# Kernel tuning notes

Measured on AMD Instinct MI355X. Metric: run time of the kernel, lower is better.

The kernel has to match this reference:

```python
import jax, jax.numpy as jnp
import numpy as np

D_MODEL = 1024
N_HEADS = 16
D_KEYS = 64
D_LLM = 4096
Q_RANK = 512
KV_RANK = 512
EPS = 1e-5


def layernorm(x, g, b):
    mu = jnp.mean(x, axis=-1, keepdims=True)
    var = jnp.mean(jnp.square(x - mu), axis=-1, keepdims=True)
    return (x - mu) * jax.lax.rsqrt(var + EPS) * g + b


def setup_inputs() -> dict:
    key = jax.random.key(0)
    ks = jax.random.split(key, 10)
    te = jax.random.normal(ks[0], (4, 1024, D_MODEL), jnp.float32)
    se = jax.random.normal(ks[1], (1000, D_LLM), jnp.float32)
    s = 0.02
    return {
        'target_embedding': te,
        'source_embedding': se,
        'value_embedding': se,  # module asserts source == value
        'q_a_w': jax.random.normal(ks[2], (Q_RANK, D_MODEL), jnp.float32) * s,
        'q_ln_g': jnp.ones((Q_RANK,), jnp.float32),
        'q_ln_b': jnp.zeros((Q_RANK,), jnp.float32),
        'q_b_w': jax.random.normal(ks[3], (N_HEADS * D_KEYS, Q_RANK), jnp.float32) * s,
        'kv_a_w': jax.random.normal(ks[4], (KV_RANK, D_LLM), jnp.float32) * s,
        'kv_ln_g': jnp.ones((KV_RANK,), jnp.float32),
        'kv_ln_b': jnp.zeros((KV_RANK,), jnp.float32),
        'kv_b_w': jax.random.normal(ks[5], (N_HEADS * 2 * D_KEYS, KV_RANK), jnp.float32) * s,
        'out_w': jax.random.normal(ks[6], (D_LLM, N_HEADS * D_KEYS), jnp.float32) * s,
        'out_b': jnp.zeros((D_LLM,), jnp.float32),
    }


def reference(target_embedding, source_embedding, value_embedding,
              q_a_w, q_ln_g, q_ln_b, q_b_w,
              kv_a_w, kv_ln_g, kv_ln_b, kv_b_w, out_w, out_b):
    B, L, _ = target_embedding.shape
    S = source_embedding.shape[0]
    # Q path: LoRA down -> LN -> up, [B,L,H,E]
    q = layernorm(target_embedding @ q_a_w.T, q_ln_g, q_ln_b) @ q_b_w.T
    q = q.reshape(B, L, N_HEADS, D_KEYS)
    # KV path (no batch dim, broadcast across B)
    ckv = layernorm(source_embedding @ kv_a_w.T, kv_ln_g, kv_ln_b)  # [S, r]
    kv = (ckv @ kv_b_w.T).reshape(S, N_HEADS, 2 * D_KEYS)
    k, v = kv[..., :D_KEYS], kv[..., D_KEYS:]  # [S,H,E] each
    scale = 1.0 / np.sqrt(D_KEYS)
    scores = jnp.einsum('blhe,she->bhls', q, k)  # [B,H,L,S]
    A = jax.nn.softmax(scale * scores, axis=-1)  # dropout inactive (eval)
    out = jnp.einsum('bhls,she->blhe', A, v).reshape(B, L, N_HEADS * D_KEYS)
    return out @ out_w.T + out_b
```

## Files before the change

kernel.cpp:

```cpp
#include <hip/hip_runtime.h>

typedef unsigned short u16;
typedef __bf16 bf16x8 __attribute__((ext_vector_type(8)));
typedef __bf16 bf16x4 __attribute__((ext_vector_type(4)));
typedef float f32x4 __attribute__((ext_vector_type(4)));

#define DEV __device__ __forceinline__

DEV u16 f2bf(float f){
  unsigned u = __float_as_uint(f);
  u += 0x7fff + ((u >> 16) & 1);
  return (u16)(u >> 16);
}
DEV float bf2f(u16 v){ return __uint_as_float(((unsigned)v) << 16); }

DEV void gll16(const void* g, void* l){
  __builtin_amdgcn_global_load_lds(
    (__attribute__((address_space(1))) unsigned int*)(unsigned long long)g,
    (__attribute__((address_space(3))) unsigned int*)(unsigned int)(unsigned long long)l,
    16, 0, 0);
}

template<int WM, int WN, int OBF, int BIAS>
__global__ __launch_bounds__(256) void gemm_bt(
    const u16* __restrict__ A, int lda, long sA1, long sA2,
    const u16* __restrict__ B, int ldb, long sB1, long sB2,
    void* __restrict__ Cv, int ldc, long sC1, long sC2,
    const float* __restrict__ bias,
    int M, int N, int K, int Z2)
{
  constexpr int BM = WM*64, BN = WN*64;
  constexpr int NW = WM*WN;
  constexpr int A_INSTS = BM/16, B_INSTS = BN/16;
  constexpr int APW = A_INSTS/NW, BPW = B_INSTS/NW;
  __shared__ u16 sA[BM*32];
  __shared__ u16 sB[BN*32];
  const int tid  = threadIdx.x;
  const int wave = tid >> 6, lane = tid & 63;
  const int quad = lane >> 4, l16 = lane & 15;
  const int wm = wave % WM, wn = wave / WM;
  const long bm = blockIdx.y, bn = blockIdx.x;
  const int z  = blockIdx.z;
  const int z1 = z / Z2, z2 = z - z1*Z2;
  const u16* Ab = A + z1*sA1 + z2*sA2 + bm*BM*(long)lda;
  const u16* Bb = B + z1*sB1 + z2*sB2 + bn*BN*(long)ldb;

  f32x4 acc[4][4] = {};

  for (int k0 = 0; k0 < K; k0 += 32){
    __syncthreads();
#pragma unroll
    for (int j = 0; j < APW; j++){
      const int inst = wave*APW + j;
      const int o = inst*1024 + lane*16;
      const int row = o >> 6, colb = o & 63;
      gll16(Ab + (long)row*lda + k0 + (colb >> 1), &sA[inst*512]);
    }
#pragma unroll
    for (int j = 0; j < BPW; j++){
      const int inst = wave*BPW + j;
      const int o = inst*1024 + lane*16;
      const int row = o >> 6, colb = o & 63;
      gll16(Bb + (long)row*ldb + k0 + (colb >> 1), &sB[inst*512]);
    }
    __syncthreads();
    bf16x8 af[4], bfr[4];
#pragma unroll
    for (int mi = 0; mi < 4; mi++)
      af[mi] = *(const bf16x8*)&sA[(wm*64 + mi*16 + l16)*32 + quad*8];
#pragma unroll
    for (int ni = 0; ni < 4; ni++)
      bfr[ni] = *(const bf16x8*)&sB[(wn*64 + ni*16 + l16)*32 + quad*8];
#pragma unroll
    for (int mi = 0; mi < 4; mi++)
#pragma unroll
      for (int ni = 0; ni < 4; ni++)
        acc[mi][ni] = __builtin_amdgcn_mfma_f32_16x16x32_bf16(af[mi], bfr[ni], acc[mi][ni], 0, 0, 0);
  }

  const long crow0 = bm*BM + wm*64 + quad*4;
  const long ccol0 = bn*BN + wn*64 + l16;
  if (OBF){
    u16* Cp = (u16*)Cv + z1*sC1 + z2*sC2;
#pragma unroll
    for (int mi = 0; mi < 4; mi++)
#pragma unroll
      for (int ni = 0; ni < 4; ni++)
#pragma unroll
        for (int r = 0; r < 4; r++)
          Cp[(crow0 + mi*16 + r)*ldc + ccol0 + ni*16] = f2bf(acc[mi][ni][r]);
  } else {
    float* Cp = (float*)Cv + z1*sC1 + z2*sC2;
    float bv[4] = {0.f,0.f,0.f,0.f};
    if (BIAS){
#pragma unroll
      for (int ni = 0; ni < 4; ni++) bv[ni] = bias[ccol0 + ni*16];
    }
#pragma unroll
    for (int mi = 0; mi < 4; mi++)
#pragma unroll
      for (int ni = 0; ni < 4; ni++)
#pragma unroll
        for (int r = 0; r < 4; r++)
          Cp[(crow0 + mi*16 + r)*ldc + ccol0 + ni*16] = acc[mi][ni][r] + bv[ni];
  }
}

__global__ __launch_bounds__(512, 2) void gemm256(
    const u16* __restrict__ A, const u16* __restrict__ B,
    float* __restrict__ C, const float* __restrict__ bias,
    int N, int K, int TN)
{
  __shared__ __align__(16) u16 sA[32768];
  __shared__ __align__(16) u16 sB[32768];
  const int tid  = threadIdx.x;
  const int w    = tid >> 6, lane = tid & 63;
  const int quad = lane >> 4, l16 = lane & 15;
  const int wm = w >> 2, wn = w & 3;
  const int cpx = gridDim.x >> 3;
  const int bid = blockIdx.x;
  const int wg  = (bid & 7)*cpx + (bid >> 3);
  const long bm = wg / TN, bn = wg % TN;
  const int NT = K >> 6;

  const int rsub = lane >> 3;
  const int kk16 = (lane & 7) ^ rsub;
  const u16* Ag = A + (bm*256 + w*8 + rsub)*(long)K + kk16*8;
  const u16* Bg = B + (bn*256 + w*8 + rsub)*(long)K + kk16*8;
  u16* dA = sA + w*512;
  u16* dB = sB + w*512;

  auto stage = [&](const u16* G, u16* D, int T){
#pragma unroll
    for (int c = 0; c < 4; c++)
      gll16(G + ((long)c*64)*K + T*64, D + c*4096);
  };

  const int xr  = l16 & 7;
  const int ko0 = ((0*4 + quad) ^ xr) * 8;
  const int ko1 = ((1*4 + quad) ^ xr) * 8;
  const u16* rA0 = sA + (wm*128 + l16)*64;
  const u16* rB0 = sB + (wn*64  + l16)*64;

  f32x4 acc[8][4] = {};
  bf16x8 aF[4][2], bF[4][2];

  stage(Ag, dA, 0);
  stage(Bg, dB, 0);
  asm volatile("s_waitcnt vmcnt(0)" ::: "memory");
  __builtin_amdgcn_s_barrier();

  for (int T = 0; T < NT; ++T){
    const int buf = T & 1;
    const u16* rA = rA0 + buf*16384;
    const u16* rB = rB0 + buf*16384;

    if (T+1 < NT){
      stage(Ag, dA + (buf^1)*16384, T+1);
      stage(Bg, dB + (buf^1)*16384, T+1);
    }

#pragma unroll
    for (int nj = 0; nj < 4; nj++){
      bF[nj][0] = *(const bf16x8*)(rB + nj*1024 + ko0);
      bF[nj][1] = *(const bf16x8*)(rB + nj*1024 + ko1);
    }
#pragma unroll
    for (int mi = 0; mi < 4; mi++){
      aF[mi][0] = *(const bf16x8*)(rA + mi*1024 + ko0);
      aF[mi][1] = *(const bf16x8*)(rA + mi*1024 + ko1);
    }
#pragma unroll
    for (int kk = 0; kk < 2; kk++)
#pragma unroll
      for (int mi = 0; mi < 4; mi++)
#pragma unroll
        for (int nj = 0; nj < 4; nj++)
          acc[mi][nj] = __builtin_amdgcn_mfma_f32_16x16x32_bf16(aF[mi][kk], bF[nj][kk], acc[mi][nj], 0,0,0);

#pragma unroll
    for (int mi = 0; mi < 4; mi++){
      aF[mi][0] = *(const bf16x8*)(rA + (4+mi)*1024 + ko0);
      aF[mi][1] = *(const bf16x8*)(rA + (4+mi)*1024 + ko1);
    }
#pragma unroll
    for (int kk = 0; kk < 2; kk++)
#pragma unroll
      for (int mi = 0; mi < 4; mi++)
#pragma unroll
        for (int nj = 0; nj < 4; nj++)
          acc[4+mi][nj] = __builtin_amdgcn_mfma_f32_16x16x32_bf16(aF[mi][kk], bF[nj][kk], acc[4+mi][nj], 0,0,0);

    asm volatile("s_waitcnt vmcnt(0)" ::: "memory");
    __syncthreads();
  }

  const long crow0 = bm*256 + wm*128 + quad*4;
  const long ccol0 = bn*256 + wn*64  + l16;
  float bv[4];
#pragma unroll
  for (int ni = 0; ni < 4; ni++) bv[ni] = bias ? bias[ccol0 + ni*16] : 0.f;
#pragma unroll
  for (int mi = 0; mi < 8; mi++)
#pragma unroll
    for (int ni = 0; ni < 4; ni++)
#pragma unroll
      for (int r = 0; r < 4; r++)
        C[(crow0 + mi*16 + r)*(long)N + ccol0 + ni*16] = acc[mi][ni][r] + bv[ni];
}

__global__ __launch_bounds__(256) void cvt_all(
    const float* __restrict__ te,   const float* __restrict__ qaw,
    const float* __restrict__ qbw,  const float* __restrict__ kvaw,
    const float* __restrict__ kvbw, const float* __restrict__ outw,
    const float* __restrict__ se,
    u16* __restrict__ te_bf, u16* __restrict__ qa_bf, u16* __restrict__ qb_bf,
    u16* __restrict__ kva_bf, u16* __restrict__ kvb_bf,
    u16* __restrict__ outw_bf, u16* __restrict__ se_bf)
{
  const long NG = 4194304;
  const float QSC = 0.18033688011f;
  for (long g = (long)blockIdx.x*256 + threadIdx.x; g < NG; g += (long)gridDim.x*256){
    const float* src; u16* dst; long rel; bool zero = false; float sc = 1.f;
    if (g < 1048576)      { src=te;   dst=te_bf;   rel=g; }
    else if (g < 1179648) { src=qaw;  dst=qa_bf;   rel=g-1048576; }
    else if (g < 1310720) { src=qbw;  dst=qb_bf;   rel=g-1179648; sc = QSC; }
    else if (g < 1835008) { src=kvaw; dst=kva_bf;  rel=g-1310720; }
    else if (g < 2097152) { src=kvbw; dst=kvb_bf;  rel=g-1835008; }
    else if (g < 3145728) { src=outw; dst=outw_bf; rel=g-2097152; }
    else                  { src=se;   dst=se_bf;   rel=g-3145728; zero = (rel>>10) >= 1000; }
    ushort4 o;
    if (!zero){
      float4 v = *(const float4*)(src + rel*4);
      o.x = f2bf(v.x*sc); o.y = f2bf(v.y*sc); o.z = f2bf(v.z*sc); o.w = f2bf(v.w*sc);
    } else { o.x = 0; o.y = 0; o.z = 0; o.w = 0; }
    *(ushort4*)(dst + rel*4) = o;
  }
}

__global__ __launch_bounds__(256) void ln_both(
    u16* __restrict__ out_q,  const float* __restrict__ in_q,
    const float* __restrict__ qg, const float* __restrict__ qb_,
    u16* __restrict__ out_kv, const float* __restrict__ in_kv,
    const float* __restrict__ kg, const float* __restrict__ kb_)
{
  long row; const float* in; u16* outp; const float* gam; const float* bet;
  int nparts; long pstride; int valid;
  if (blockIdx.x < 4096){
    row = blockIdx.x; in = in_q; outp = out_q; gam = qg; bet = qb_;
    nparts = 2; pstride = 4096L*512; valid = 1;
  } else {
    row = blockIdx.x - 4096; in = in_kv; outp = out_kv; gam = kg; bet = kb_;
    nparts = 8; pstride = 1024L*512; valid = (row < 1000);
  }
  const int tid = threadIdx.x;
  u16* op = outp + row*512 + tid*2;
  if (!valid){
    ushort2 z; z.x = 0; z.y = 0;
    *(ushort2*)op = z;
    return;
  }
  float2 x; x.x = 0.f; x.y = 0.f;
  for (int p = 0; p < nparts; p++){
    float2 v = *(const float2*)(in + p*pstride + row*512 + tid*2);
    x.x += v.x; x.y += v.y;
  }
  float s  = x.x + x.y;
  float s2 = x.x*x.x + x.y*x.y;
#pragma unroll
  for (int m = 32; m; m >>= 1){ s += __shfl_xor(s, m, 64); s2 += __shfl_xor(s2, m, 64); }
  __shared__ float red[8];
  const int wave = tid >> 6, lane = tid & 63;
  if (lane == 0){ red[wave*2] = s; red[wave*2+1] = s2; }
  __syncthreads();
  float ts = red[0]+red[2]+red[4]+red[6];
  float t2 = red[1]+red[3]+red[5]+red[7];
  float mu  = ts * (1.f/512.f);
  float var = t2 * (1.f/512.f) - mu*mu;
  float rs  = rsqrtf(var + 1e-5f);
  float2 g2 = *(const float2*)(gam + tid*2);
  float2 b2 = *(const float2*)(bet + tid*2);
  ushort2 o;
  o.x = f2bf((x.x - mu)*rs*g2.x + b2.x);
  o.y = f2bf((x.y - mu)*rs*g2.y + b2.y);
  *(ushort2*)op = o;
}

__global__ __launch_bounds__(256) void split_kv(
    const float* __restrict__ kv, u16* __restrict__ kbf, u16* __restrict__ vT)
{
  const int h  = blockIdx.x;
  const int sc = blockIdx.y;
  const int s0 = sc*64;
  const long PST = 1024L*2048;
  __shared__ u16 tile[64][65];
  const int e  = threadIdx.x & 63;
  const int sg = threadIdx.x >> 6;
#pragma unroll
  for (int i = 0; i < 16; i++){
    const int sl = i*4 + sg;
    const int s = s0 + sl;
    float kvl = kv[(long)s*2048 + h*128 + e]      + kv[PST + (long)s*2048 + h*128 + e];
    float vvl = kv[(long)s*2048 + h*128 + 64 + e] + kv[PST + (long)s*2048 + h*128 + 64 + e];
    kbf[((long)h*1024 + s)*64 + ((e + 8*s) & 63)] = f2bf(kvl);
    tile[sl][e] = f2bf(vvl);
  }
  __syncthreads();
#pragma unroll
  for (int i = 0; i < 16; i++){
    const int er = i*4 + sg;
    const int s  = s0 + e;
    const int t128 = s >> 7, pos = s & 127;
    vT[(((long)h*8 + t128)*64 + er)*128 + ((pos + 8*er) & 127)] = tile[e][er];
  }
}

__global__ __launch_bounds__(256) void flash_attn(
    const u16* __restrict__ Q, const u16* __restrict__ Kt,
    const u16* __restrict__ Vt, u16* __restrict__ O)
{
  __shared__ u16 sK[128*64];
  __shared__ u16 sV[64*128];
  __shared__ u16 sPT[128*136];
  const int tid = threadIdx.x, w = tid >> 6, lane = tid & 63;
  const int quad = lane >> 4, l16 = lane & 15;
  const int h = blockIdx.y;
  const long q0 = (long)blockIdx.x * 128;

  bf16x8 bq[2][2];
#pragma unroll
  for (int ni = 0; ni < 2; ni++)
#pragma unroll
    for (int kf = 0; kf < 2; kf++)
      bq[ni][kf] = *(const bf16x8*)&Q[(q0 + w*32 + ni*16 + l16)*1024 + h*64 + kf*32 + quad*8];

  f32x4 accO[2][4] = {};
  float lst[2] = {0.f, 0.f};

#pragma unroll
  for (int j = 0; j < 4; j++){
    const int inst = w*4 + j;
    gll16(Kt + (long)h*65536 + inst*512 + lane*8, &sK[inst*512]);
  }
  __syncthreads();

  for (int it = 0; it < 8; it++){
#pragma unroll
    for (int j = 0; j < 4; j++){
      const int inst = w*4 + j;
      gll16(Vt + ((long)(h*8 + it))*8192 + inst*512 + lane*8, &sV[inst*512]);
    }

    f32x4 accS[8][2] = {};
#pragma unroll
    for (int kf = 0; kf < 2; kf++)
#pragma unroll
      for (int mi = 0; mi < 8; mi++){
        const int sr = mi*16 + l16;
        bf16x8 ka = *(const bf16x8*)&sK[sr*64 + ((kf*32 + quad*8 + 8*sr) & 63)];
#pragma unroll
        for (int ni = 0; ni < 2; ni++)
          accS[mi][ni] = __builtin_amdgcn_mfma_f32_16x16x32_bf16(ka, bq[ni][kf], accS[mi][ni], 0, 0, 0);
      }

    __syncthreads();

    if (it < 7){
      const long kb = (long)h*65536 + (long)(it+1)*8192;
#pragma unroll
      for (int j = 0; j < 4; j++){
        const int inst = w*4 + j;
        gll16(Kt + kb + inst*512 + lane*8, &sK[inst*512]);
      }
    }

#pragma unroll
    for (int ni = 0; ni < 2; ni++){
      if (it == 7){
#pragma unroll
        for (int mi = 0; mi < 8; mi++)
#pragma unroll
          for (int r = 0; r < 4; r++){
            const int s = 896 + mi*16 + quad*4 + r;
            if (s >= 1000) accS[mi][ni][r] = -3e38f;
          }
      }
      float sum = 0.f;
      const int qloc = w*32 + ni*16 + l16;
#pragma unroll
      for (int mi = 0; mi < 8; mi++){
        float p0 = exp2f(accS[mi][ni][0]);
        float p1 = exp2f(accS[mi][ni][1]);
        float p2 = exp2f(accS[mi][ni][2]);
        float p3 = exp2f(accS[mi][ni][3]);
        sum += (p0 + p1) + (p2 + p3);
        bf16x4 pk;
        pk[0] = (__bf16)p0; pk[1] = (__bf16)p1;
        pk[2] = (__bf16)p2; pk[3] = (__bf16)p3;
        *(bf16x4*)&sPT[qloc*136 + mi*16 + quad*4] = pk;
      }
      sum += __shfl_xor(sum, 16, 64);
      sum += __shfl_xor(sum, 32, 64);
      lst[ni] += sum;
    }

#pragma unroll
    for (int kf = 0; kf < 4; kf++){
      bf16x8 pa[2], vb[4];
#pragma unroll
      for (int mi = 0; mi < 2; mi++)
        pa[mi] = *(const bf16x8*)&sPT[(w*32 + mi*16 + l16)*136 + kf*32 + quad*8];
#pragma unroll
      for (int ni = 0; ni < 4; ni++){
        const int e = ni*16 + l16;
        vb[ni] = *(const bf16x8*)&sV[e*128 + ((kf*32 + quad*8 + 8*e) & 127)];
      }
#pragma unroll
      for (int mi = 0; mi < 2; mi++)
#pragma unroll
        for (int ni = 0; ni < 4; ni++)
          accO[mi][ni] = __builtin_amdgcn_mfma_f32_16x16x32_bf16(pa[mi], vb[ni], accO[mi][ni], 0, 0, 0);
    }
    __syncthreads();
  }

#pragma unroll
  for (int mi = 0; mi < 2; mi++){
    f32x4 l4;
#pragma unroll
    for (int r = 0; r < 4; r++) l4[r] = __shfl(lst[mi], quad*4 + r, 64);
#pragma unroll
    for (int ni = 0; ni < 4; ni++)
#pragma unroll
      for (int r = 0; r < 4; r++)
        O[(q0 + w*32 + mi*16 + quad*4 + r)*1024 + h*64 + ni*16 + l16] =
            f2bf(accO[mi][ni][r] / l4[r]);
  }
}

extern "C" void kernel_launch(void* const* d_in, const int* in_sizes, int n_in,
                              void* d_out, int out_size, void* d_ws, size_t ws_size,
                              hipStream_t stream)
{
  const float* te   = (const float*)d_in[0];
  const float* se   = (const float*)d_in[1];
  const float* qaw  = (const float*)d_in[3];
  const float* qlg  = (const float*)d_in[4];
  const float* qlb  = (const float*)d_in[5];
  const float* qbw  = (const float*)d_in[6];
  const float* kvaw = (const float*)d_in[7];
  const float* kvlg = (const float*)d_in[8];
  const float* kvlb = (const float*)d_in[9];
  const float* kvbw = (const float*)d_in[10];
  const float* outw = (const float*)d_in[11];
  const float* outb = (const float*)d_in[12];
  float* out = (float*)d_out;
  (void)ws_size; (void)in_sizes; (void)n_in; (void)out_size;

  char* ws = (char*)d_ws;
  const size_t MB = 1024*1024;
  u16*   te_bf  = (u16*)  (ws + 0*MB);
  u16*   se_bf  = (u16*)  (ws + 8*MB);
  float* qlat   = (float*)(ws + 16*MB);
  float* ckvp   = (float*)(ws + 32*MB);
  float* kvf    = (float*)(ws + 48*MB);
  u16*   qa_bf   = (u16*)(ws + 64*MB);
  u16*   qb_bf   = (u16*)(ws + 65*MB);
  u16*   kva_bf  = (u16*)(ws + 66*MB);
  u16*   kvb_bf  = (u16*)(ws + 70*MB);
  u16*   outw_bf = (u16*)(ws + 72*MB);
  u16*   qln_bf  = (u16*)(ws + 80*MB);
  u16*   q_bf    = (u16*)(ws + 84*MB);
  u16*   ckv_bf  = (u16*)(ws + 92*MB);
  u16*   k_bf    = (u16*)(ws + 93*MB);
  u16*   vT_bf   = (u16*)(ws + 95*MB);
  u16*   attn_bf = (u16*)(ws + 97*MB);

  cvt_all<<<4096, 256, 0, stream>>>(
      te, qaw, qbw, kvaw, kvbw, outw, se,
      te_bf, qa_bf, qb_bf, kva_bf, kvb_bf, outw_bf, se_bf);

  gemm_bt<2,2,0,0><<<dim3(4, 32, 2), 256, 0, stream>>>(
      te_bf, 1024, 512, 0, qa_bf, 1024, 512, 0,
      qlat, 512, 4096L*512, 0, nullptr, 4096, 512, 512, 1);
  gemm_bt<2,2,0,0><<<dim3(4, 8, 8), 256, 0, stream>>>(
      se_bf, 4096, 512, 0, kva_bf, 4096, 512, 0,
      ckvp, 512, 1024L*512, 0, nullptr, 1024, 512, 512, 1);
  ln_both<<<4096 + 1024, 256, 0, stream>>>(
      qln_bf, qlat, qlg, qlb, ckv_bf, ckvp, kvlg, kvlb);
  gemm_bt<2,2,1,0><<<dim3(8, 32, 1), 256, 0, stream>>>(
      qln_bf, 512, 0,0, qb_bf, 512, 0,0, q_bf, 1024, 0,0, nullptr, 4096, 1024, 512, 1);
  gemm_bt<2,2,0,0><<<dim3(16, 8, 2), 256, 0, stream>>>(
      ckv_bf, 512, 256, 0, kvb_bf, 512, 256, 0,
      kvf, 2048, 1024L*2048, 0, nullptr, 1024, 2048, 256, 1);
  split_kv<<<dim3(16, 16), 256, 0, stream>>>(kvf, k_bf, vT_bf);

  flash_attn<<<dim3(32, 16), 256, 0, stream>>>(q_bf, k_bf, vT_bf, attn_bf);

  gemm256<<<dim3(256), 512, 0, stream>>>(
      attn_bf, outw_bf, out, outb, 4096, 1024, 16);
}
```

Before: 299.0 us.

## Pipeline gemm256 with four-stage K=32 LDS ring and prefetch depth two

Reworks the 256x256 GEMM main loop from a double-buffered K=64 tile to a four-slot ring of K=32 tiles with two tiles in flight. Waits use partial vmcnt counts so the next tile's loads overlap compute. The LDS swizzle is changed to fit the narrower rows, and MFMA sections are wrapped in s_setprio. The aim is to hide global-to-LDS latency and reduce barrier stalls, at the cost of more barriers per K and fragile waitcnt bookkeeping.

```diff
diff --git a/kernel.cpp b/kernel.cpp
--- a/kernel.cpp
+++ b/kernel.cpp
@@ -121,78 +121,67 @@
   const int bid = blockIdx.x;
   const int wg  = (bid & 7)*cpx + (bid >> 3);
   const long bm = wg / TN, bn = wg % TN;
-  const int NT = K >> 6;
-
-  const int rsub = lane >> 3;
-  const int kk16 = (lane & 7) ^ rsub;
-  const u16* Ag = A + (bm*256 + w*8 + rsub)*(long)K + kk16*8;
-  const u16* Bg = B + (bn*256 + w*8 + rsub)*(long)K + kk16*8;
-  u16* dA = sA + w*512;
-  u16* dB = sB + w*512;
-
-  auto stage = [&](const u16* G, u16* D, int T){
-#pragma unroll
-    for (int c = 0; c < 4; c++)
-      gll16(G + ((long)c*64)*K + T*64, D + c*4096);
+  const int NS = K >> 5;
+
+  const int rsub = lane >> 2;
+  const int kk16 = (lane & 3) ^ (rsub & 3) ^ ((lane >> 4) & 3);
+  const u16* Ag = A + (bm*256 + w*32 + rsub)*(long)K + kk16*8;
+  const u16* Bg = B + (bn*256 + w*32 + rsub)*(long)K + kk16*8;
+  u16* dA = sA + w*1024;
+  u16* dB = sB + w*1024;
+
+  auto stage = [&](int b, int t){
+    const long koff = (long)t*32;
+#pragma unroll
+    for (int j = 0; j < 2; j++){
+      gll16(Ag + (long)(j*16)*K + koff, dA + b*8192 + j*512);
+      gll16(Bg + (long)(j*16)*K + koff, dB + b*8192 + j*512);
+    }
   };
 
-  const int xr  = l16 & 7;
-  const int ko0 = ((0*4 + quad) ^ xr) * 8;
-  const int ko1 = ((1*4 + quad) ^ xr) * 8;
-  const u16* rA0 = sA + (wm*128 + l16)*64;
-  const u16* rB0 = sB + (wn*64  + l16)*64;
+  const int ko = (quad ^ (l16 & 3) ^ ((l16 >> 2) & 3)) * 8;
+  const u16* rA0 = sA + (wm*128 + l16)*32;
+  const u16* rB0 = sB + (wn*64  + l16)*32;
 
   f32x4 acc[8][4] = {};
-  bf16x8 aF[4][2], bF[4][2];
-
-  stage(Ag, dA, 0);
-  stage(Bg, dB, 0);
-  asm volatile("s_waitcnt vmcnt(0)" ::: "memory");
+
+  stage(0, 0);
+  stage(1, 1);
+  asm volatile("s_waitcnt vmcnt(4)" ::: "memory");
   __builtin_amdgcn_s_barrier();
 
-  for (int T = 0; T < NT; ++T){
-    const int buf = T & 1;
-    const u16* rA = rA0 + buf*16384;
-    const u16* rB = rB0 + buf*16384;
-
-    if (T+1 < NT){
-      stage(Ag, dA + (buf^1)*16384, T+1);
-      stage(Bg, dB + (buf^1)*16384, T+1);
-    }
-
-#pragma unroll
-    for (int nj = 0; nj < 4; nj++){
-      bF[nj][0] = *(const bf16x8*)(rB + nj*1024 + ko0);
-      bF[nj][1] = *(const bf16x8*)(rB + nj*1024 + ko1);
-    }
-#pragma unroll
-    for (int mi = 0; mi < 4; mi++){
-      aF[mi][0] = *(const bf16x8*)(rA + mi*1024 + ko0);
-      aF[mi][1] = *(const bf16x8*)(rA + mi*1024 + ko1);
-    }
-#pragma unroll
-    for (int kk = 0; kk < 2; kk++)
-#pragma unroll
-      for (int mi = 0; mi < 4; mi++)
-#pragma unroll
-        for (int nj = 0; nj < 4; nj++)
-          acc[mi][nj] = __builtin_amdgcn_mfma_f32_16x16x32_bf16(aF[mi][kk], bF[nj][kk], acc[mi][nj], 0,0,0);
-
-#pragma unroll
-    for (int mi = 0; mi < 4; mi++){
-      aF[mi][0] = *(const bf16x8*)(rA + (4+mi)*1024 + ko0);
-      aF[mi][1] = *(const bf16x8*)(rA + (4+mi)*1024 + ko1);
-    }
-#pragma unroll
-    for (int kk = 0; kk < 2; kk++)
-#pragma unroll
-      for (int mi = 0; mi < 4; mi++)
-#pragma unroll
-        for (int nj = 0; nj < 4; nj++)
-          acc[4+mi][nj] = __builtin_amdgcn_mfma_f32_16x16x32_bf16(aF[mi][kk], bF[nj][kk], acc[4+mi][nj], 0,0,0);
-
-    asm volatile("s_waitcnt vmcnt(0)" ::: "memory");
-    __syncthreads();
+  for (int t = 0; t < NS; ++t){
+    const int b = t & 3;
+    if (t+2 < NS) stage((t+2) & 3, t+2);
+
+    const u16* rA = rA0 + b*8192;
+    const u16* rB = rB0 + b*8192;
+    bf16x8 aF[8], bF[4];
+#pragma unroll
+    for (int ni = 0; ni < 4; ni++)
+      bF[ni] = *(const bf16x8*)(rB + ni*512 + ko);
+#pragma unroll
+    for (int mi = 0; mi < 8; mi++)
+      aF[mi] = *(const bf16x8*)(rA + mi*512 + ko);
+
+    __builtin_amdgcn_s_setprio(1);
+#pragma unroll
+    for (int mi = 0; mi < 8; mi++)
+#pragma unroll
+      for (int ni = 0; ni < 4; ni++)
+        acc[mi][ni] = __builtin_amdgcn_mfma_f32_16x16x32_bf16(aF[mi], bF[ni], acc[mi][ni], 0,0,0);
+    __builtin_amdgcn_s_setprio(0);
+
+    if (t+3 < NS){
+      asm volatile("s_waitcnt vmcnt(4)" ::: "memory");
+      __builtin_amdgcn_s_barrier();
+    } else if (t+2 == NS){
+      asm volatile("s_waitcnt vmcnt(0)" ::: "memory");
+      __builtin_amdgcn_s_barrier();
+    } else if (t+3 == NS){
+      asm volatile("s_waitcnt vmcnt(4)" ::: "memory");
+      __builtin_amdgcn_s_barrier();
+    }
   }
 
   const long crow0 = bm*256 + wm*128 + quad*4;
```

Result: no change. 303.7 us (+1.6%).
